# Kernel tuning notes

Measured on AMD Instinct MI355X. Metric: run time of the kernel, lower is better.

The kernel has to match this reference:

```python
import jax, jax.numpy as jnp
import numpy as np

B, C_IN, C_OUT, H, W = 8, 32, 32, 256, 256
M1H, M2H = 32, 32  # modes1//2, modes2//2 (dilate=1)
WSCALE = 0.02      # ~xavier-ish scale for weights


def setup_inputs() -> dict:
    key = jax.random.key(0)
    ks = jax.random.split(key, 6)
    wshape = (C_IN, C_OUT, M1H, M2H)
    return {
        "x": jax.random.normal(ks[0], (B, C_IN, H, W), jnp.float32),
        "w1r": jax.random.normal(ks[1], wshape, jnp.float32) * WSCALE,
        "w1i": jax.random.normal(ks[2], wshape, jnp.float32) * WSCALE,
        "w2r": jax.random.normal(ks[3], wshape, jnp.float32) * WSCALE,
        "w2i": jax.random.normal(ks[4], wshape, jnp.float32) * WSCALE,
        "bias": jax.random.normal(ks[5], (1, C_OUT, 1, 1), jnp.float32),
    }


def reference(x, w1r, w1i, w2r, w2i, bias):
    # complex spectral weights (torch.view_as_complex equivalent)
    w1 = w1r + 1j * w1i  # [I, O, m1h, m2h]
    w2 = w2r + 1j * w2i
    b, c, h, w = x.shape
    x_ft = jnp.fft.rfft2(x)  # [B, I, H, W//2+1] complex64
    # mode-truncated complex channel mixing on low-frequency corners
    out_lo = jnp.einsum('bixy,ioxy->boxy', x_ft[:, :, :M1H, :M2H], w1)
    out_hi = jnp.einsum('bixy,ioxy->boxy', x_ft[:, :, -M1H:, :M2H], w2)
    out_ft = jnp.zeros((b, w1.shape[1], h, w // 2 + 1), jnp.complex64)
    out_ft = out_ft.at[:, :, :M1H, :M2H].set(out_lo)
    out_ft = out_ft.at[:, :, -M1H:, :M2H].set(out_hi)
    out = jnp.fft.irfft2(out_ft, s=(h, w))  # [B, O, H, W] float32
    return out + bias
```

## Files before the change

kernel.cpp:

```cpp
#include <hip/hip_runtime.h>
#include <hip/hip_bf16.h>


#define BD 256

typedef __attribute__((ext_vector_type(8))) short bf16x8;
typedef __attribute__((ext_vector_type(4))) float f32x4;

__device__ inline unsigned short f2bf(float f) {
    union { float f; unsigned u; } v; v.f = f;
    unsigned r = v.u + 0x7FFF + ((v.u >> 16) & 1);
    return (unsigned short)(r >> 16);
}

__global__ void k_setup(float2* __restrict__ tw,
                        unsigned short* __restrict__ BmA, unsigned short* __restrict__ BmC,
                        unsigned short* __restrict__ Tm, unsigned short* __restrict__ Th,
                        const float* __restrict__ w1r, const float* __restrict__ w1i,
                        const float* __restrict__ w2r, const float* __restrict__ w2i,
                        float2* __restrict__ wpack) {
    __shared__ float Tr[64][65];
    __shared__ float Ti[64][65];
    int b = blockIdx.x, t = threadIdx.x;
    if (b == 0) {
        double th = 6.283185307179586476925286766559 * (double)t / 256.0;
        tw[t] = make_float2((float)cos(th), (float)sin(th));
    } else if (b <= 128) {
        int idx = (b - 1) * BD + t;
        if (idx < 16384) {
            int w = idx & 255, n = idx >> 8;
            int ky = n >> 1, c = n & 1;
            double th = 6.283185307179586476925286766559 * (double)((ky * w) & 255) / 256.0;
            BmA[idx] = f2bf(c ? (float)(-sin(th)) : (float)cos(th));
        } else {
            int j = idx - 16384;
            int k = j & 63, w = j >> 6;
            int ky = k >> 1, c = k & 1;
            double th = 6.283185307179586476925286766559 * (double)((ky * w) & 255) / 256.0;
            BmC[j] = f2bf(c ? (float)(-sin(th)) : (float)cos(th));
        }
    } else if (b <= 256) {
        int idx = (b - 129) * BD + t;
        int h = idx & 255, n2 = idx >> 8;
        int j = n2 >> 1, c = n2 & 1;
        int kx = (j < 32) ? j : j + 192;
        double th = 6.283185307179586476925286766559 * (double)((kx * h) & 255) / 256.0;
        Tm[idx] = f2bf(c ? (float)(-sin(th)) : (float)cos(th));
    } else if (b <= 384) {
        int idx = (b - 257) * BD + t;
        int k2 = idx & 127, h = idx >> 7;
        int m = k2 >> 1, c = k2 & 1;
        int kx = (m < 32) ? m : m + 192;
        double th = 6.283185307179586476925286766559 * (double)((kx * h) & 255) / 256.0;
        Th[idx] = f2bf(c ? (float)(-sin(th)) : (float)cos(th));
    } else {
        int blk = b - 385;
        int half = blk >> 8;
        int tile = blk & 255;
        int tr = tile >> 4, tc = tile & 15;
        int io0 = tr * 64, cm0 = tc * 64;
        const float* wr = half ? w2r : w1r;
        const float* wi = half ? w2i : w1i;
        int rr = t >> 2, c0 = (t & 3) * 16;
        {
            const float4* srcr = (const float4*)(wr + (long)(io0 + rr) * 1024 + cm0 + c0);
            const float4* srci = (const float4*)(wi + (long)(io0 + rr) * 1024 + cm0 + c0);
#pragma unroll
            for (int p = 0; p < 4; ++p) {
                float4 vr = srcr[p], vi = srci[p];
                int cc = c0 + p * 4;
                Tr[rr][cc + 0] = vr.x; Tr[rr][cc + 1] = vr.y; Tr[rr][cc + 2] = vr.z; Tr[rr][cc + 3] = vr.w;
                Ti[rr][cc + 0] = vi.x; Ti[rr][cc + 1] = vi.y; Ti[rr][cc + 2] = vi.z; Ti[rr][cc + 3] = vi.w;
            }
        }
        __syncthreads();
        {
            int cm = cm0 + rr;
            int ky = cm & 31;
            float s = (ky == 0 ? 1.0f : 2.0f) * (1.0f / 65536.0f);
            float2* dst = wpack + ((long)(half * 1024 + cm)) * 1024 + io0 + c0;
#pragma unroll
            for (int k = 0; k < 16; ++k)
                dst[k] = make_float2(Tr[c0 + k][rr] * s, Ti[c0 + k][rr] * s);
        }
    }
}

__global__ __launch_bounds__(512) void k_fftA(const float* __restrict__ x,
                                              const unsigned short* __restrict__ BmA,
                                              const unsigned short* __restrict__ Tm,
                                              float2* __restrict__ Z) {
    __shared__ __align__(16) unsigned short Ybt[64 * 264];
    __shared__ __align__(16) char buf[64 * 264 * 2];
    unsigned short* As = (unsigned short*)buf;
    float* ZZs = (float*)buf;
    int t = threadIdx.x, bi = blockIdx.x;
    int wv = t >> 6, lane = t & 63, lm = lane & 15, quad = lane >> 4;
    int nst = (wv >> 1) * 16, mh = wv & 1;
    bf16x8 bfr[8];
#pragma unroll
    for (int kk = 0; kk < 8; ++kk)
        bfr[kk] = *(const bf16x8*)&BmA[(nst + lm) * 256 + kk * 32 + quad * 8];
    int sr = t >> 3, sc = (t & 7) * 32;
    for (int c = 0; c < 4; ++c) {
        {
            const float* xp = x + ((long)bi * 256 + c * 64 + sr) * 256 + sc;
            unsigned short* dst = &As[sr * 264 + sc];
#pragma unroll
            for (int j = 0; j < 8; ++j) {
                float4 v = *(const float4*)(xp + j * 4);
                ushort4 bq;
                bq.x = f2bf(v.x); bq.y = f2bf(v.y); bq.z = f2bf(v.z); bq.w = f2bf(v.w);
                *(ushort4*)(dst + j * 4) = bq;
            }
        }
        __syncthreads();
        f32x4 acc0 = {}, acc1 = {};
#pragma unroll
        for (int kk = 0; kk < 8; ++kk) {
            bf16x8 af0 = *(const bf16x8*)&As[(mh * 32 + lm) * 264 + kk * 32 + quad * 8];
            bf16x8 af1 = *(const bf16x8*)&As[(mh * 32 + 16 + lm) * 264 + kk * 32 + quad * 8];
            acc0 = __builtin_amdgcn_mfma_f32_16x16x32_bf16(af0, bfr[kk], acc0, 0, 0, 0);
            acc1 = __builtin_amdgcn_mfma_f32_16x16x32_bf16(af1, bfr[kk], acc1, 0, 0, 0);
        }
        {
            ushort4 w0, w1;
            w0.x = f2bf(acc0[0]); w0.y = f2bf(acc0[1]); w0.z = f2bf(acc0[2]); w0.w = f2bf(acc0[3]);
            w1.x = f2bf(acc1[0]); w1.y = f2bf(acc1[1]); w1.z = f2bf(acc1[2]); w1.w = f2bf(acc1[3]);
            int base = (nst + lm) * 264 + c * 64 + mh * 32 + quad * 4;
            *(ushort4*)&Ybt[base] = w0;
            *(ushort4*)&Ybt[base + 16] = w1;
        }
        __syncthreads();
    }
    bf16x8 afr[8];
#pragma unroll
    for (int kk = 0; kk < 8; ++kk)
        afr[kk] = *(const bf16x8*)&Tm[(wv * 16 + lm) * 256 + kk * 32 + quad * 8];
    f32x4 az[4] = {};
#pragma unroll
    for (int kk = 0; kk < 8; ++kk)
#pragma unroll
        for (int nt = 0; nt < 4; ++nt) {
            bf16x8 bf = *(const bf16x8*)&Ybt[(nt * 16 + lm) * 264 + kk * 32 + quad * 8];
            az[nt] = __builtin_amdgcn_mfma_f32_16x16x32_bf16(afr[kk], bf, az[nt], 0, 0, 0);
        }
#pragma unroll
    for (int nt = 0; nt < 4; ++nt)
#pragma unroll
        for (int r = 0; r < 4; ++r)
            ZZs[(wv * 16 + quad * 4 + r) * 65 + nt * 16 + lm] = az[nt][r];
    __syncthreads();
#pragma unroll
    for (int p = 0; p < 4; ++p) {
        int cid = p * 512 + t;
        int m = cid >> 5, ky = cid & 31;
        float zr = ZZs[(2 * m) * 65 + 2 * ky]     - ZZs[(2 * m + 1) * 65 + 2 * ky + 1];
        float zi = ZZs[(2 * m) * 65 + 2 * ky + 1] + ZZs[(2 * m + 1) * 65 + 2 * ky];
        Z[(long)bi * 2048 + cid] = make_float2(zr, zi);
    }
}

__global__ void k_mix(const float2* __restrict__ Z, const float2* __restrict__ wpack,
                      float2* __restrict__ Zmix) {
    __shared__ float2 Ws[4][1024];
    __shared__ float2 Zs[256][4];
    __shared__ float2 Os[256][4];
    int t = threadIdx.x;
    int mk0 = blockIdx.x * 4;
    {
        const float4* src = (const float4*)(wpack + (long)mk0 * 1024);
        float4* dst = (float4*)&Ws[0][0];
        for (int j = t; j < 2048; j += BD) dst[j] = src[j];
    }
    for (int j = t; j < 512; j += BD) {
        int bi = j >> 1, p = j & 1;
        *(float4*)&Zs[bi][p * 2] = *(const float4*)&Z[(long)bi * 2048 + mk0 + p * 2];
    }
    __syncthreads();
    int o = t & 31, kk = (t >> 5) & 3, bh = t >> 7;
    float ar[4], ai[4];
#pragma unroll
    for (int j = 0; j < 4; ++j) { ar[j] = 0.f; ai[j] = 0.f; }
    for (int i = 0; i < 32; ++i) {
        float2 w = Ws[kk][i * 32 + o];
#pragma unroll
        for (int j = 0; j < 4; ++j) {
            float2 z = Zs[(bh * 4 + j) * 32 + i][kk];
            ar[j] = fmaf(z.x, w.x, fmaf(-z.y, w.y, ar[j]));
            ai[j] = fmaf(z.x, w.y, fmaf( z.y, w.x, ai[j]));
        }
    }
#pragma unroll
    for (int j = 0; j < 4; ++j)
        Os[(bh * 4 + j) * 32 + o][kk] = make_float2(ar[j], ai[j]);
    __syncthreads();
    for (int j = t; j < 512; j += BD) {
        int row = j >> 1, p = j & 1;
        *(float4*)&Zmix[(long)row * 2048 + mk0 + p * 2] = *(float4*)&Os[row][p * 2];
    }
}

__global__ __launch_bounds__(512) void k_fftC(const float2* __restrict__ Zmix,
                                              const unsigned short* __restrict__ Th,
                                              const unsigned short* __restrict__ BmC,
                                              const float* __restrict__ bias,
                                              float* __restrict__ out) {
    __shared__ __align__(16) unsigned short Gs[128 * 72];
    __shared__ __align__(16) char buf[128 * 72 * 2];
    unsigned short* Bz = (unsigned short*)buf;
    unsigned short* Bsh = (unsigned short*)buf;
    int t = threadIdx.x;
    int bo = blockIdx.x >> 1, hb = blockIdx.x & 1;
    {
#pragma unroll
        for (int p = 0; p < 4; ++p) {
            int cid = p * 512 + t;
            int m = cid >> 5, ky = cid & 31;
            float2 z = Zmix[(long)bo * 2048 + cid];
            unsigned short zr = f2bf(z.x), zi = f2bf(z.y), nzr = f2bf(-z.x);
            Bz[(2 * ky) * 136 + 2 * m]         = zr;
            Bz[(2 * ky) * 136 + 2 * m + 1]     = zi;
            Bz[(2 * ky + 1) * 136 + 2 * m]     = zi;
            Bz[(2 * ky + 1) * 136 + 2 * m + 1] = nzr;
        }
    }
    __syncthreads();
    int wv = t >> 6, lane = t & 63, lm = lane & 15, quad = lane >> 4;
    {
        bf16x8 afr[4];
#pragma unroll
        for (int kk = 0; kk < 4; ++kk)
            afr[kk] = *(const bf16x8*)&Th[(hb * 128 + wv * 16 + lm) * 128 + kk * 32 + quad * 8];
        f32x4 ag[4] = {};
#pragma unroll
        for (int kk = 0; kk < 4; ++kk)
#pragma unroll
            for (int nt = 0; nt < 4; ++nt) {
                bf16x8 bf = *(const bf16x8*)&Bz[(nt * 16 + lm) * 136 + kk * 32 + quad * 8];
                ag[nt] = __builtin_amdgcn_mfma_f32_16x16x32_bf16(afr[kk], bf, ag[nt], 0, 0, 0);
            }
#pragma unroll
        for (int nt = 0; nt < 4; ++nt)
#pragma unroll
            for (int r = 0; r < 4; ++r)
                Gs[(wv * 16 + quad * 4 + r) * 72 + nt * 16 + lm] = f2bf(ag[nt][r]);
    }
    __syncthreads();
    bf16x8 a0 = *(const bf16x8*)&Gs[(wv * 16 + lm) * 72 + quad * 8];
    bf16x8 a1 = *(const bf16x8*)&Gs[(wv * 16 + lm) * 72 + 32 + quad * 8];
    float bv = bias[bo & 31];
    long rowbase = (long)bo * 256 + hb * 128 + wv * 16;
    for (int p = 0; p < 2; ++p) {
        if (p) __syncthreads();
        {
            int w = t >> 2, k0 = (t & 3) * 16;
            const uint4* src = (const uint4*)(BmC + (p * 128 + w) * 64 + k0);
            *(uint4*)&Bsh[w * 72 + k0]     = src[0];
            *(uint4*)&Bsh[w * 72 + k0 + 8] = src[1];
        }
        __syncthreads();
        f32x4 acc[8] = {};
#pragma unroll
        for (int nt = 0; nt < 8; ++nt) {
            bf16x8 b0 = *(const bf16x8*)&Bsh[(nt * 16 + lm) * 72 + quad * 8];
            bf16x8 b1 = *(const bf16x8*)&Bsh[(nt * 16 + lm) * 72 + 32 + quad * 8];
            acc[nt] = __builtin_amdgcn_mfma_f32_16x16x32_bf16(a0, b0, acc[nt], 0, 0, 0);
            acc[nt] = __builtin_amdgcn_mfma_f32_16x16x32_bf16(a1, b1, acc[nt], 0, 0, 0);
        }
#pragma unroll
        for (int nt = 0; nt < 8; ++nt)
#pragma unroll
            for (int r = 0; r < 4; ++r)
                out[(rowbase + quad * 4 + r) * 256 + p * 128 + nt * 16 + lm] = acc[nt][r] + bv;
    }
}

extern "C" void kernel_launch(void* const* d_in, const int* in_sizes, int n_in,
                              void* d_out, int out_size, void* d_ws, size_t ws_size,
                              hipStream_t stream) {
    const float* x    = (const float*)d_in[0];
    const float* w1r  = (const float*)d_in[1];
    const float* w1i  = (const float*)d_in[2];
    const float* w2r  = (const float*)d_in[3];
    const float* w2i  = (const float*)d_in[4];
    const float* bias = (const float*)d_in[5];

    char* ws = (char*)d_ws;
    float2* tw             = (float2*)(ws);
    float2* wpack          = (float2*)(ws + 4096);
    unsigned short* BmA    = (unsigned short*)(ws + 4096 + (16l << 20));
    unsigned short* BmC    = BmA + 64 * 256;
    unsigned short* Tm     = (unsigned short*)(ws + 4096 + (16l << 20) + 65536);
    unsigned short* Th     = Tm + 128 * 256;
    float2* Z              = (float2*)(ws + 4096 + (16l << 20) + 65536 + 131072);
    float2* Zmix           = (float2*)((char*)Z + (4l << 20));
    float* out             = (float*)d_out;

    k_setup <<<897, BD, 0, stream>>>(tw, BmA, BmC, Tm, Th, w1r, w1i, w2r, w2i, wpack);
    k_fftA  <<<256, 512, 0, stream>>>(x, BmA, Tm, Z);
    k_mix   <<<512, BD, 0, stream>>>(Z, wpack, Zmix);
    k_fftC  <<<512, 512, 0, stream>>>(Zmix, Th, BmC, bias, out);
}
```

Before: 165.1 us.

## Split forward FFT over row halves and store mixed spectrum as bf16

```diff
diff --git a/kernel.cpp b/kernel.cpp
--- a/kernel.cpp
+++ b/kernel.cpp
@@ -90,11 +90,11 @@
                                               const unsigned short* __restrict__ BmA,
                                               const unsigned short* __restrict__ Tm,
                                               float2* __restrict__ Z) {
-    __shared__ __align__(16) unsigned short Ybt[64 * 264];
+    __shared__ __align__(16) unsigned short Ybt[64 * 136];
     __shared__ __align__(16) char buf[64 * 264 * 2];
     unsigned short* As = (unsigned short*)buf;
     float* ZZs = (float*)buf;
-    int t = threadIdx.x, bi = blockIdx.x;
+    int t = threadIdx.x, bi = blockIdx.x >> 1, hh2 = blockIdx.x & 1;
     int wv = t >> 6, lane = t & 63, lm = lane & 15, quad = lane >> 4;
     int nst = (wv >> 1) * 16, mh = wv & 1;
     bf16x8 bfr[8];
@@ -102,9 +102,9 @@
     for (int kk = 0; kk < 8; ++kk)
         bfr[kk] = *(const bf16x8*)&BmA[(nst + lm) * 256 + kk * 32 + quad * 8];
     int sr = t >> 3, sc = (t & 7) * 32;
-    for (int c = 0; c < 4; ++c) {
-        {
-            const float* xp = x + ((long)bi * 256 + c * 64 + sr) * 256 + sc;
+    for (int c = 0; c < 2; ++c) {
+        {
+            const float* xp = x + ((long)bi * 256 + hh2 * 128 + c * 64 + sr) * 256 + sc;
             unsigned short* dst = &As[sr * 264 + sc];
 #pragma unroll
             for (int j = 0; j < 8; ++j) {
@@ -127,22 +127,22 @@
             ushort4 w0, w1;
             w0.x = f2bf(acc0[0]); w0.y = f2bf(acc0[1]); w0.z = f2bf(acc0[2]); w0.w = f2bf(acc0[3]);
             w1.x = f2bf(acc1[0]); w1.y = f2bf(acc1[1]); w1.z = f2bf(acc1[2]); w1.w = f2bf(acc1[3]);
-            int base = (nst + lm) * 264 + c * 64 + mh * 32 + quad * 4;
+            int base = (nst + lm) * 136 + c * 64 + mh * 32 + quad * 4;
             *(ushort4*)&Ybt[base] = w0;
             *(ushort4*)&Ybt[base + 16] = w1;
         }
         __syncthreads();
     }
-    bf16x8 afr[8];
-#pragma unroll
-    for (int kk = 0; kk < 8; ++kk)
-        afr[kk] = *(const bf16x8*)&Tm[(wv * 16 + lm) * 256 + kk * 32 + quad * 8];
+    bf16x8 afr[4];
+#pragma unroll
+    for (int kk = 0; kk < 4; ++kk)
+        afr[kk] = *(const bf16x8*)&Tm[(wv * 16 + lm) * 256 + hh2 * 128 + kk * 32 + quad * 8];
     f32x4 az[4] = {};
 #pragma unroll
-    for (int kk = 0; kk < 8; ++kk)
+    for (int kk = 0; kk < 4; ++kk)
 #pragma unroll
         for (int nt = 0; nt < 4; ++nt) {
-            bf16x8 bf = *(const bf16x8*)&Ybt[(nt * 16 + lm) * 264 + kk * 32 + quad * 8];
+            bf16x8 bf = *(const bf16x8*)&Ybt[(nt * 16 + lm) * 136 + kk * 32 + quad * 8];
             az[nt] = __builtin_amdgcn_mfma_f32_16x16x32_bf16(afr[kk], bf, az[nt], 0, 0, 0);
         }
 #pragma unroll
@@ -157,12 +157,12 @@
         int m = cid >> 5, ky = cid & 31;
         float zr = ZZs[(2 * m) * 65 + 2 * ky]     - ZZs[(2 * m + 1) * 65 + 2 * ky + 1];
         float zi = ZZs[(2 * m) * 65 + 2 * ky + 1] + ZZs[(2 * m + 1) * 65 + 2 * ky];
-        Z[(long)bi * 2048 + cid] = make_float2(zr, zi);
+        Z[(long)(hh2 * 256 + bi) * 2048 + cid] = make_float2(zr, zi);
     }
 }
 
 __global__ void k_mix(const float2* __restrict__ Z, const float2* __restrict__ wpack,
-                      float2* __restrict__ Zmix) {
+                      unsigned* __restrict__ Zmixb) {
     __shared__ float2 Ws[4][1024];
     __shared__ float2 Zs[256][4];
     __shared__ float2 Os[256][4];
@@ -175,7 +175,11 @@
     }
     for (int j = t; j < 512; j += BD) {
         int bi = j >> 1, p = j & 1;
-        *(float4*)&Zs[bi][p * 2] = *(const float4*)&Z[(long)bi * 2048 + mk0 + p * 2];
+        float4 a = *(const float4*)&Z[(long)bi * 2048 + mk0 + p * 2];
+        float4 b = *(const float4*)&Z[(long)(256 + bi) * 2048 + mk0 + p * 2];
+        float4 s;
+        s.x = a.x + b.x; s.y = a.y + b.y; s.z = a.z + b.z; s.w = a.w + b.w;
+        *(float4*)&Zs[bi][p * 2] = s;
     }
     __syncthreads();
     int o = t & 31, kk = (t >> 5) & 3, bh = t >> 7;
@@ -197,11 +201,15 @@
     __syncthreads();
     for (int j = t; j < 512; j += BD) {
         int row = j >> 1, p = j & 1;
-        *(float4*)&Zmix[(long)row * 2048 + mk0 + p * 2] = *(float4*)&Os[row][p * 2];
-    }
-}
-
-__global__ __launch_bounds__(512) void k_fftC(const float2* __restrict__ Zmix,
+        float2 a = Os[row][p * 2], b2 = Os[row][p * 2 + 1];
+        uint2 u;
+        u.x = (unsigned)f2bf(a.x)  | ((unsigned)f2bf(a.y)  << 16);
+        u.y = (unsigned)f2bf(b2.x) | ((unsigned)f2bf(b2.y) << 16);
+        *(uint2*)&Zmixb[(long)row * 2048 + mk0 + p * 2] = u;
+    }
+}
+
+__global__ __launch_bounds__(512) void k_fftC(const unsigned* __restrict__ Zmixb,
                                               const unsigned short* __restrict__ Th,
                                               const unsigned short* __restrict__ BmC,
                                               const float* __restrict__ bias,
@@ -217,8 +225,10 @@
         for (int p = 0; p < 4; ++p) {
             int cid = p * 512 + t;
             int m = cid >> 5, ky = cid & 31;
-            float2 z = Zmix[(long)bo * 2048 + cid];
-            unsigned short zr = f2bf(z.x), zi = f2bf(z.y), nzr = f2bf(-z.x);
+            unsigned z = Zmixb[(long)bo * 2048 + cid];
+            unsigned short zr = (unsigned short)z;
+            unsigned short zi = (unsigned short)(z >> 16);
+            unsigned short nzr = zr ^ 0x8000;
             Bz[(2 * ky) * 136 + 2 * m]         = zr;
             Bz[(2 * ky) * 136 + 2 * m + 1]     = zi;
             Bz[(2 * ky + 1) * 136 + 2 * m]     = zi;
@@ -294,11 +304,11 @@
     unsigned short* Tm     = (unsigned short*)(ws + 4096 + (16l << 20) + 65536);
     unsigned short* Th     = Tm + 128 * 256;
     float2* Z              = (float2*)(ws + 4096 + (16l << 20) + 65536 + 131072);
-    float2* Zmix           = (float2*)((char*)Z + (4l << 20));
+    unsigned* Zmixb        = (unsigned*)((char*)Z + (8l << 20));
     float* out             = (float*)d_out;
 
     k_setup <<<897, BD, 0, stream>>>(tw, BmA, BmC, Tm, Th, w1r, w1i, w2r, w2i, wpack);
-    k_fftA  <<<256, 512, 0, stream>>>(x, BmA, Tm, Z);
-    k_mix   <<<512, BD, 0, stream>>>(Z, wpack, Zmix);
-    k_fftC  <<<512, 512, 0, stream>>>(Zmix, Th, BmC, bias, out);
-}
+    k_fftA  <<<512, 512, 0, stream>>>(x, BmA, Tm, Z);
+    k_mix   <<<512, BD, 0, stream>>>(Z, wpack, Zmixb);
+    k_fftC  <<<512, 512, 0, stream>>>(Zmixb, Th, BmC, bias, out);
+}
```

After: 169.1 us. 1.02x slower.
